# Kernel tuning notes

Hardware: AMD Instinct MI355X
Metric: run time of the kernel (lower is better)

The kernel has to match this reference:

```python
import jax, jax.numpy as jnp
import numpy as np

BETA = 0.25  # commitment cost (original code's undefined self.betas)


def setup_inputs() -> dict:
    key = jax.random.key(0)
    k1, k2 = jax.random.split(key)
    B, D, H, W = 32, 256, 32, 32
    K = 1024
    x = jax.random.normal(k1, (B, D, H, W), dtype=jnp.float32)
    # nn.Embedding init: uniform(-1/K, 1/K)
    emb = jax.random.uniform(k2, (K, D), dtype=jnp.float32,
                             minval=-1.0 / K, maxval=1.0 / K)
    return {"x": x, "emb": emb}


def reference(x, emb):
    # x: [B, D, H, W] -> NHWC
    xp = jnp.transpose(x, (0, 2, 3, 1))          # [B, H, W, D]
    D = emb.shape[1]
    z = xp.reshape(-1, D)                        # [N, D]
    # pairwise squared distance: ||z||^2 + ||e||^2 - 2 z e^T
    dist = (jnp.sum(z * z, axis=1, keepdims=True)
            + jnp.sum(emb * emb, axis=1)
            - 2.0 * jnp.einsum('nd,kd->nk', z, emb))  # [N, K]
    idx = jnp.argmin(dist, axis=1)               # [N] int
    z_quant = emb[idx].reshape(xp.shape)         # [B, H, W, D]
    sg = jax.lax.stop_gradient
    loss = (jnp.mean((sg(z_quant) - xp) ** 2)
            + BETA * jnp.mean((z_quant - sg(xp)) ** 2))
    # straight-through estimator
    z_quant = xp + sg(z_quant - xp)
    z_quant = jnp.transpose(z_quant, (0, 3, 1, 2))  # back to NCHW
    return z_quant, idx, loss
```

## Files before the change

### kernel.cpp

```cpp
#include <hip/hip_runtime.h>

typedef _Float16 half8 __attribute__((ext_vector_type(8)));
typedef _Float16 half4v __attribute__((ext_vector_type(4)));
typedef float f32x4 __attribute__((ext_vector_type(4)));

#define ZQ_ELEMS 8388608
#define N_TOK    32768
#define D_DIM    256
#define K_CB     1024

#define FLAG_CAP 32768
#define ESCALE   1024.0f
#define TAU      0.15f

__device__ __align__(16) _Float16 g_eh[K_CB * D_DIM];
__device__ float g_ck[K_CB];
__device__ float g_bk[K_CB];
__device__ float g_loss;
__device__ int   g_cnt;
__device__ int   g_flags[FLAG_CAP];

__global__ __launch_bounds__(256) void vq_prep(const float* __restrict__ emb) {
  const int tid = threadIdx.x;
  const int w   = tid >> 6;
  const int l   = tid & 63;
  const int k   = (blockIdx.x << 2) + w;
  f32x4 v = *(const f32x4*)(emb + (k << 8) + (l << 2));
  double sd = (double)v[0]*v[0] + (double)v[1]*v[1] + (double)v[2]*v[2] + (double)v[3]*v[3];
  #pragma unroll
  for (int m = 1; m < 64; m <<= 1) sd += __shfl_xor(sd, m);
  if (l == 0) { g_bk[k] = (float)sd; g_ck[k] = 512.0f * (float)sd; }
  half4v h;
  h[0] = (_Float16)(v[0] * ESCALE); h[1] = (_Float16)(v[1] * ESCALE);
  h[2] = (_Float16)(v[2] * ESCALE); h[3] = (_Float16)(v[3] * ESCALE);
  *(half4v*)(g_eh + (k << 8) + (l << 2)) = h;
  if (blockIdx.x == 0 && tid == 0) { g_loss = 0.0f; g_cnt = 0; }
}

__global__ __launch_bounds__(256, 2) void vq_main(const float* __restrict__ x,
                                                  const float* __restrict__ emb,
                                                  float* __restrict__ out) {
  __shared__ __align__(16) _Float16 zt[64 * 256];
  __shared__ float ckl[K_CB];
  __shared__ float wv1[4][64], wv2[4][64];
  __shared__ int   wi1[4][64];
  __shared__ int   fidx[64];
  __shared__ float lred[4];

  const int tid = threadIdx.x;
  const int n0  = blockIdx.x * 64;
  const int b   = blockIdx.x >> 4;
  const int hw0 = (blockIdx.x & 15) << 6;

  #pragma unroll
  for (int i = 0; i < 4; i++) ckl[tid + 256 * i] = g_ck[tid + 256 * i];

  {
    const int hw8 = (tid & 7) << 3;
    const int dl  = tid >> 3;
    #pragma unroll
    for (int it = 0; it < 8; it++) {
      const int d = (it << 5) + dl;
      const float* src = x + (((b << 8) + d) << 10) + hw0 + hw8;
      f32x4 a0 = *(const f32x4*)src;
      f32x4 a1 = *(const f32x4*)(src + 4);
      _Float16 cv[8];
      cv[0]=(_Float16)a0[0]; cv[1]=(_Float16)a0[1]; cv[2]=(_Float16)a0[2]; cv[3]=(_Float16)a0[3];
      cv[4]=(_Float16)a1[0]; cv[5]=(_Float16)a1[1]; cv[6]=(_Float16)a1[2]; cv[7]=(_Float16)a1[3];
      const int blkx = d >> 3;
      #pragma unroll
      for (int i = 0; i < 8; i++) {
        const int n   = hw8 + i;
        const int blk = blkx ^ i ^ (tid & 7);
        zt[(n << 8) + (blk << 3) + (d & 7)] = cv[i];
      }
    }
  }
  __syncthreads();

  const int w = tid >> 6;
  const int l = tid & 63;
  const int c = l & 15;
  const int q = l >> 4;

  half8 af[4][8];
  #pragma unroll
  for (int t = 0; t < 4; t++) {
    const int n  = (t << 4) + c;
    const int sw = (n & 7) ^ (n >> 3);
    #pragma unroll
    for (int s = 0; s < 8; s++) {
      const int K = (s << 2) + q;
      af[t][s] = *(const half8*)(zt + (n << 8) + ((K ^ sw) << 3));
    }
  }

  float v1[4][4], v2[4][4]; int i1[4][4];
  #pragma unroll
  for (int t = 0; t < 4; t++)
    #pragma unroll
    for (int r = 0; r < 4; r++) { v1[t][r] = -3e38f; v2[t][r] = -3e38f; i1[t][r] = 0; }

  for (int jj = 0; jj < 16; jj++) {
    const int k0 = (w << 4) + (jj << 6);
    const float ckv = ckl[k0 + c];
    f32x4 acc[4];
    #pragma unroll
    for (int t = 0; t < 4; t++) acc[t] = f32x4{-ckv, -ckv, -ckv, -ckv};
    #pragma unroll
    for (int s = 0; s < 8; s++) {
      const half8 bf = *(const half8*)(g_eh + ((k0 + c) << 8) + (s << 5) + (q << 3));
      #pragma unroll
      for (int t = 0; t < 4; t++)
        acc[t] = __builtin_amdgcn_mfma_f32_16x16x32_f16(af[t][s], bf, acc[t], 0, 0, 0);
    }
    const int kk = k0 + c;
    #pragma unroll
    for (int t = 0; t < 4; t++)
      #pragma unroll
      for (int r = 0; r < 4; r++) {
        const float sv = acc[t][r];
        if (sv > v1[t][r]) { v2[t][r] = v1[t][r]; v1[t][r] = sv; i1[t][r] = kk; }
        else if (sv > v2[t][r]) v2[t][r] = sv;
      }
  }

  #pragma unroll
  for (int t = 0; t < 4; t++)
    #pragma unroll
    for (int r = 0; r < 4; r++) {
      float a1v = v1[t][r], a2v = v2[t][r]; int ai = i1[t][r];
      #pragma unroll
      for (int m = 8; m >= 1; m >>= 1) {
        const float o1 = __shfl_xor(a1v, m);
        const int   oi = __shfl_xor(ai, m);
        const float o2 = __shfl_xor(a2v, m);
        if (o1 > a1v || (o1 == a1v && oi < ai)) { a2v = fmaxf(a1v, o2); a1v = o1; ai = oi; }
        else a2v = fmaxf(a2v, o1);
      }
      if (c == 0) {
        const int nl = (t << 4) + (q << 2) + r;
        wv1[w][nl] = a1v; wv2[w][nl] = a2v; wi1[w][nl] = ai;
      }
    }
  __syncthreads();

  if (tid < 64) {
    float a1v = wv1[0][tid], a2v = wv2[0][tid]; int ai = wi1[0][tid];
    #pragma unroll
    for (int ww = 1; ww < 4; ww++) {
      const float o1 = wv1[ww][tid]; const int oi = wi1[ww][tid]; const float o2 = wv2[ww][tid];
      if (o1 > a1v || (o1 == a1v && oi < ai)) { a2v = fmaxf(a1v, o2); a1v = o1; ai = oi; }
      else a2v = fmaxf(a2v, o1);
    }
    fidx[tid] = ai;
    out[ZQ_ELEMS + n0 + tid] = (float)ai;
    if (a1v - a2v < TAU) {
      int p = atomicAdd(&g_cnt, 1);
      if (p < FLAG_CAP) g_flags[p] = n0 + tid;
    }
  }
  __syncthreads();

  float lacc = 0.0f;
  {
    const int hw = tid & 63;
    const int sw = (hw & 7) ^ (hw >> 3);
    const float* erow = emb + (fidx[hw] << 8);
    #pragma unroll
    for (int it = 0; it < 8; it++) {
      const int dblk = (it << 2) + w;
      half8 zv = *(const half8*)(zt + (hw << 8) + ((dblk ^ sw) << 3));
      f32x4 e0 = *(const f32x4*)(erow + (dblk << 3));
      f32x4 e1 = *(const f32x4*)(erow + (dblk << 3) + 4);
      #pragma unroll
      for (int j = 0; j < 8; j++) {
        const int d = (dblk << 3) + j;
        const float ef = (j < 4) ? e0[j] : e1[j - 4];
        const float df = ef - (float)zv[j];
        lacc += df * df;
        out[(((b << 8) + d) << 10) + hw0 + hw] = ef;
      }
    }
  }
  #pragma unroll
  for (int m = 1; m < 64; m <<= 1) lacc += __shfl_xor(lacc, m);
  if (l == 0) lred[w] = lacc;
  __syncthreads();
  if (tid == 0) atomicAdd(&g_loss, lred[0] + lred[1] + lred[2] + lred[3]);
}

#define FIX_G 8
__global__ __launch_bounds__(256) void vq_fix(const float* __restrict__ x,
                                              const float* __restrict__ emb,
                                              float* __restrict__ out) {
  __shared__ float zl[FIX_G][256];
  __shared__ float aA[FIX_G];
  __shared__ int   tkn[FIX_G];
  __shared__ float bvv[FIX_G][256];
  __shared__ int   bkk[FIX_G][256];
  const int tid = threadIdx.x;
  int cnt = g_cnt; if (cnt > FLAG_CAP) cnt = FLAG_CAP;
  const int ngrp = (cnt + FIX_G - 1) / FIX_G;
  for (int grp = blockIdx.x; grp < ngrp; grp += gridDim.x) {
    const int base = grp * FIX_G;
    if (tid < FIX_G) {
      const int s = base + tid;
      tkn[tid] = (s < cnt) ? g_flags[s] : g_flags[0];
    }
    __syncthreads();
    #pragma unroll
    for (int g = 0; g < FIX_G; g++) {
      const int n = tkn[g];
      const int b = n >> 10, hw = n & 1023;
      zl[g][tid] = x[(((b << 8) + tid) << 10) + hw];
    }
    __syncthreads();
    {
      const int g = tid >> 5, l32 = tid & 31;
      double s = 0.0;
      #pragma unroll
      for (int j = 0; j < 8; j++) { const double z = (double)zl[g][(l32 << 3) + j]; s += z * z; }
      #pragma unroll
      for (int m = 1; m < 32; m <<= 1) s += __shfl_xor(s, m);
      if (l32 == 0) aA[g] = (float)s;
    }
    __syncthreads();
    float bv[FIX_G]; int bk[FIX_G];
    #pragma unroll
    for (int g = 0; g < FIX_G; g++) { bv[g] = 3.4e38f; bk[g] = 0; }
    for (int r = 0; r < 4; r++) {
      const int k = (r << 8) + tid;
      const f32x4* er = (const f32x4*)(emb + (k << 8));
      double c[FIX_G];
      #pragma unroll
      for (int g = 0; g < FIX_G; g++) c[g] = 0.0;
      for (int d4 = 0; d4 < 64; d4++) {
        const f32x4 ev = er[d4];
        #pragma unroll
        for (int j = 0; j < 4; j++) {
          const double e = (double)ev[j];
          const int d = (d4 << 2) + j;
          #pragma unroll
          for (int g = 0; g < FIX_G; g++) c[g] = fma(e, (double)zl[g][d], c[g]);
        }
      }
      const float bkv = g_bk[k];
      #pragma unroll
      for (int g = 0; g < FIX_G; g++) {
        const float c32 = (float)c[g];
        const float T = aA[g] + bkv;
        const float D = T - 2.0f * c32;
        if (D < bv[g]) { bv[g] = D; bk[g] = k; }
      }
    }
    #pragma unroll
    for (int g = 0; g < FIX_G; g++) { bvv[g][tid] = bv[g]; bkk[g][tid] = bk[g]; }
    for (int sh = 7; sh >= 0; sh--) {
      const int off = 1 << sh;
      __syncthreads();
      for (int idx = tid; idx < (FIX_G << sh); idx += 256) {
        const int g = idx >> sh, j = idx & (off - 1);
        const float v2c = bvv[g][j + off]; const int k2 = bkk[g][j + off];
        if (v2c < bvv[g][j] || (v2c == bvv[g][j] && k2 < bkk[g][j])) {
          bvv[g][j] = v2c; bkk[g][j] = k2;
        }
      }
    }
    __syncthreads();
    if (tid < FIX_G && base + tid < cnt) out[ZQ_ELEMS + tkn[tid]] = (float)bkk[tid][0];
    __syncthreads();
  }
}

__global__ void vq_fin(float* __restrict__ out) {
  out[ZQ_ELEMS + N_TOK] = g_loss * (1.25f / 8388608.0f);
}

extern "C" void kernel_launch(void* const* d_in, const int* in_sizes, int n_in,
                              void* d_out, int out_size, void* d_ws, size_t ws_size,
                              hipStream_t stream) {
  const float* x   = (const float*)d_in[0];
  const float* emb = (const float*)d_in[1];
  float* out = (float*)d_out;
  vq_prep<<<256, 256, 0, stream>>>(emb);
  vq_main<<<512, 256, 0, stream>>>(x, emb, out);
  vq_fix<<<320, 256, 0, stream>>>(x, emb, out);
  vq_fin<<<1, 1, 0, stream>>>(out);
}
```

Before: 247.3 us.

## Process one flagged token per block in vq_fix with more blocks

The fp64 recheck kernel now handles one flagged token per block iteration instead of groups of eight. Each thread computes four codebook dot products at once, and the block uses a simpler tree reduction. The grid grows from 320 to 1024 blocks to spread the flagged tokens more widely. This trades codebook reuse across grouped tokens for more parallelism and lower register and shared-memory use per block. Codebook rows are now re-read once for every token rather than once per group of eight.

```diff
diff --git a/kernel.cpp b/kernel.cpp
--- a/kernel.cpp
+++ b/kernel.cpp
@@ -190,85 +190,69 @@
   if (tid == 0) atomicAdd(&g_loss, lred[0] + lred[1] + lred[2] + lred[3]);
 }
 
-#define FIX_G 8
 __global__ __launch_bounds__(256) void vq_fix(const float* __restrict__ x,
                                               const float* __restrict__ emb,
                                               float* __restrict__ out) {
-  __shared__ float zl[FIX_G][256];
-  __shared__ float aA[FIX_G];
-  __shared__ int   tkn[FIX_G];
-  __shared__ float bvv[FIX_G][256];
-  __shared__ int   bkk[FIX_G][256];
+  __shared__ float zl[256];
+  __shared__ float aA;
+  __shared__ float bvv[256];
+  __shared__ int   bkk[256];
   const int tid = threadIdx.x;
   int cnt = g_cnt; if (cnt > FLAG_CAP) cnt = FLAG_CAP;
-  const int ngrp = (cnt + FIX_G - 1) / FIX_G;
-  for (int grp = blockIdx.x; grp < ngrp; grp += gridDim.x) {
-    const int base = grp * FIX_G;
-    if (tid < FIX_G) {
-      const int s = base + tid;
-      tkn[tid] = (s < cnt) ? g_flags[s] : g_flags[0];
-    }
-    __syncthreads();
-    #pragma unroll
-    for (int g = 0; g < FIX_G; g++) {
-      const int n = tkn[g];
-      const int b = n >> 10, hw = n & 1023;
-      zl[g][tid] = x[(((b << 8) + tid) << 10) + hw];
-    }
-    __syncthreads();
+  for (int s = blockIdx.x; s < cnt; s += gridDim.x) {
+    const int n = g_flags[s];
+    const int b = n >> 10, hw = n & 1023;
+    zl[tid] = x[(((b << 8) + tid) << 10) + hw];
+    __syncthreads();
+    if (tid < 32) {
+      double sa = 0.0;
+      #pragma unroll
+      for (int j = 0; j < 8; j++) { const double z = (double)zl[(tid << 3) + j]; sa += z * z; }
+      #pragma unroll
+      for (int m = 1; m < 32; m <<= 1) sa += __shfl_xor(sa, m);
+      if (tid == 0) aA = (float)sa;
+    }
+    __syncthreads();
+    const f32x4* er0 = (const f32x4*)(emb + ((0 << 8) + tid) * 256);
+    const f32x4* er1 = (const f32x4*)(emb + ((1 << 8) + tid) * 256);
+    const f32x4* er2 = (const f32x4*)(emb + ((2 << 8) + tid) * 256);
+    const f32x4* er3 = (const f32x4*)(emb + ((3 << 8) + tid) * 256);
+    double c0 = 0.0, c1 = 0.0, c2 = 0.0, c3 = 0.0;
+    for (int d4 = 0; d4 < 64; d4++) {
+      const f32x4 e0 = er0[d4], e1 = er1[d4], e2 = er2[d4], e3 = er3[d4];
+      #pragma unroll
+      for (int j = 0; j < 4; j++) {
+        const double z = (double)zl[(d4 << 2) + j];
+        c0 = fma((double)e0[j], z, c0);
+        c1 = fma((double)e1[j], z, c1);
+        c2 = fma((double)e2[j], z, c2);
+        c3 = fma((double)e3[j], z, c3);
+      }
+    }
+    const float A = aA;
+    float bv = 3.4e38f; int bk = 0;
     {
-      const int g = tid >> 5, l32 = tid & 31;
-      double s = 0.0;
-      #pragma unroll
-      for (int j = 0; j < 8; j++) { const double z = (double)zl[g][(l32 << 3) + j]; s += z * z; }
-      #pragma unroll
-      for (int m = 1; m < 32; m <<= 1) s += __shfl_xor(s, m);
-      if (l32 == 0) aA[g] = (float)s;
-    }
-    __syncthreads();
-    float bv[FIX_G]; int bk[FIX_G];
-    #pragma unroll
-    for (int g = 0; g < FIX_G; g++) { bv[g] = 3.4e38f; bk[g] = 0; }
-    for (int r = 0; r < 4; r++) {
-      const int k = (r << 8) + tid;
-      const f32x4* er = (const f32x4*)(emb + (k << 8));
-      double c[FIX_G];
-      #pragma unroll
-      for (int g = 0; g < FIX_G; g++) c[g] = 0.0;
-      for (int d4 = 0; d4 < 64; d4++) {
-        const f32x4 ev = er[d4];
-        #pragma unroll
-        for (int j = 0; j < 4; j++) {
-          const double e = (double)ev[j];
-          const int d = (d4 << 2) + j;
-          #pragma unroll
-          for (int g = 0; g < FIX_G; g++) c[g] = fma(e, (double)zl[g][d], c[g]);
+      const float D0 = (A + g_bk[tid])        - 2.0f * (float)c0;
+      const float D1 = (A + g_bk[256 + tid])  - 2.0f * (float)c1;
+      const float D2 = (A + g_bk[512 + tid])  - 2.0f * (float)c2;
+      const float D3 = (A + g_bk[768 + tid])  - 2.0f * (float)c3;
+      if (D0 < bv) { bv = D0; bk = tid; }
+      if (D1 < bv) { bv = D1; bk = 256 + tid; }
+      if (D2 < bv) { bv = D2; bk = 512 + tid; }
+      if (D3 < bv) { bv = D3; bk = 768 + tid; }
+    }
+    bvv[tid] = bv; bkk[tid] = bk;
+    __syncthreads();
+    for (int off = 128; off >= 1; off >>= 1) {
+      if (tid < off) {
+        const float v2c = bvv[tid + off]; const int k2 = bkk[tid + off];
+        if (v2c < bvv[tid] || (v2c == bvv[tid] && k2 < bkk[tid])) {
+          bvv[tid] = v2c; bkk[tid] = k2;
         }
       }
-      const float bkv = g_bk[k];
-      #pragma unroll
-      for (int g = 0; g < FIX_G; g++) {
-        const float c32 = (float)c[g];
-        const float T = aA[g] + bkv;
-        const float D = T - 2.0f * c32;
-        if (D < bv[g]) { bv[g] = D; bk[g] = k; }
-      }
-    }
-    #pragma unroll
-    for (int g = 0; g < FIX_G; g++) { bvv[g][tid] = bv[g]; bkk[g][tid] = bk[g]; }
-    for (int sh = 7; sh >= 0; sh--) {
-      const int off = 1 << sh;
       __syncthreads();
-      for (int idx = tid; idx < (FIX_G << sh); idx += 256) {
-        const int g = idx >> sh, j = idx & (off - 1);
-        const float v2c = bvv[g][j + off]; const int k2 = bkk[g][j + off];
-        if (v2c < bvv[g][j] || (v2c == bvv[g][j] && k2 < bkk[g][j])) {
-          bvv[g][j] = v2c; bkk[g][j] = k2;
-        }
-      }
-    }
-    __syncthreads();
-    if (tid < FIX_G && base + tid < cnt) out[ZQ_ELEMS + tkn[tid]] = (float)bkk[tid][0];
+    }
+    if (tid == 0) out[ZQ_ELEMS + n] = (float)bkk[0];
     __syncthreads();
   }
 }
@@ -285,6 +269,6 @@
   float* out = (float*)d_out;
   vq_prep<<<256, 256, 0, stream>>>(emb);
   vq_main<<<512, 256, 0, stream>>>(x, emb, out);
-  vq_fix<<<320, 256, 0, stream>>>(x, emb, out);
+  vq_fix<<<1024, 256, 0, stream>>>(x, emb, out);
   vq_fin<<<1, 1, 0, stream>>>(out);
 }
```

After: 362.3 us. +46.5%, slower.

## Transpose codebook for coalesced fp64 rescoring and shrink fix groups to two tokens

Applied to the files above, without the earlier changes.

Adds a kernel that transposes the fp32 codebook into a d-major global buffer. The flagged-token fp64 rescoring kernel then reads codebook columns with coalesced per-thread loads instead of strided row reads. It processes two tokens per block instead of eight, across 512 blocks instead of 320, giving more parallelism for small flag counts at the cost of re-reading the codebook more often. This adds an extra launch and a 1 MB transposed buffer.

```diff
diff --git a/kernel.cpp b/kernel.cpp
--- a/kernel.cpp
+++ b/kernel.cpp
@@ -14,6 +14,7 @@
 #define TAU      0.15f
 
 __device__ __align__(16) _Float16 g_eh[K_CB * D_DIM];
+__device__ __align__(16) float g_ebT[D_DIM * K_CB];
 __device__ float g_ck[K_CB];
 __device__ float g_bk[K_CB];
 __device__ float g_loss;
@@ -35,6 +36,24 @@
   h[2] = (_Float16)(v[2] * ESCALE); h[3] = (_Float16)(v[3] * ESCALE);
   *(half4v*)(g_eh + (k << 8) + (l << 2)) = h;
   if (blockIdx.x == 0 && tid == 0) { g_loss = 0.0f; g_cnt = 0; }
+}
+
+__global__ __launch_bounds__(256) void vq_tr(const float* __restrict__ emb) {
+  __shared__ float tl[64][65];
+  const int tx = threadIdx.x & 63, ty = threadIdx.x >> 6;
+  const int k0 = (blockIdx.x & 15) << 6;
+  const int d0 = (blockIdx.x >> 4) << 6;
+  #pragma unroll
+  for (int j = 0; j < 16; j++) {
+    const int kk = (ty << 4) + j;
+    tl[kk][tx] = emb[((k0 + kk) << 8) + d0 + tx];
+  }
+  __syncthreads();
+  #pragma unroll
+  for (int j = 0; j < 16; j++) {
+    const int dd = (ty << 4) + j;
+    g_ebT[((d0 + dd) << 10) + k0 + tx] = tl[tx][dd];
+  }
 }
 
 __global__ __launch_bounds__(256, 2) void vq_main(const float* __restrict__ x,
@@ -190,85 +209,77 @@
   if (tid == 0) atomicAdd(&g_loss, lred[0] + lred[1] + lred[2] + lred[3]);
 }
 
-#define FIX_G 8
 __global__ __launch_bounds__(256) void vq_fix(const float* __restrict__ x,
-                                              const float* __restrict__ emb,
                                               float* __restrict__ out) {
-  __shared__ float zl[FIX_G][256];
-  __shared__ float aA[FIX_G];
-  __shared__ int   tkn[FIX_G];
-  __shared__ float bvv[FIX_G][256];
-  __shared__ int   bkk[FIX_G][256];
+  __shared__ float zt2[2][256];
+  __shared__ float aA2[2];
+  __shared__ float bvv[2][256];
+  __shared__ int   bkk[2][256];
+  __shared__ int   nn[2];
   const int tid = threadIdx.x;
   int cnt = g_cnt; if (cnt > FLAG_CAP) cnt = FLAG_CAP;
-  const int ngrp = (cnt + FIX_G - 1) / FIX_G;
+  const int ngrp = (cnt + 1) >> 1;
   for (int grp = blockIdx.x; grp < ngrp; grp += gridDim.x) {
-    const int base = grp * FIX_G;
-    if (tid < FIX_G) {
-      const int s = base + tid;
-      tkn[tid] = (s < cnt) ? g_flags[s] : g_flags[0];
-    }
-    __syncthreads();
-    #pragma unroll
-    for (int g = 0; g < FIX_G; g++) {
-      const int n = tkn[g];
-      const int b = n >> 10, hw = n & 1023;
-      zl[g][tid] = x[(((b << 8) + tid) << 10) + hw];
-    }
-    __syncthreads();
-    {
-      const int g = tid >> 5, l32 = tid & 31;
-      double s = 0.0;
-      #pragma unroll
-      for (int j = 0; j < 8; j++) { const double z = (double)zl[g][(l32 << 3) + j]; s += z * z; }
-      #pragma unroll
-      for (int m = 1; m < 32; m <<= 1) s += __shfl_xor(s, m);
-      if (l32 == 0) aA[g] = (float)s;
-    }
-    __syncthreads();
-    float bv[FIX_G]; int bk[FIX_G];
-    #pragma unroll
-    for (int g = 0; g < FIX_G; g++) { bv[g] = 3.4e38f; bk[g] = 0; }
+    const int n0 = grp << 1;
+    if (tid < 2) nn[tid] = g_flags[(n0 + tid < cnt) ? (n0 + tid) : (cnt - 1)];
+    __syncthreads();
+    #pragma unroll
+    for (int g = 0; g < 2; g++) {
+      const int n = nn[g], b = n >> 10, hw = n & 1023;
+      zt2[g][tid] = x[(((b << 8) + tid) << 10) + hw];
+    }
+    __syncthreads();
+    if (tid < 128 && (tid & 63) < 32) {
+      const int g = tid >> 6, l32 = tid & 31;
+      double sa = 0.0;
+      #pragma unroll
+      for (int j = 0; j < 8; j++) { const double z = (double)zt2[g][(l32 << 3) + j]; sa += z * z; }
+      #pragma unroll
+      for (int m = 1; m < 32; m <<= 1) sa += __shfl_xor(sa, m);
+      if (l32 == 0) aA2[g] = (float)sa;
+    }
+    __syncthreads();
+    double c0[4] = {0.0, 0.0, 0.0, 0.0};
+    double c1[4] = {0.0, 0.0, 0.0, 0.0};
+    #pragma unroll 4
+    for (int d = 0; d < 256; d++) {
+      const float* col = g_ebT + (d << 10);
+      const double z0 = (double)zt2[0][d];
+      const double z1 = (double)zt2[1][d];
+      #pragma unroll
+      for (int r = 0; r < 4; r++) {
+        const double e = (double)col[(r << 8) + tid];
+        c0[r] = fma(e, z0, c0[r]);
+        c1[r] = fma(e, z1, c1[r]);
+      }
+    }
+    const float A0 = aA2[0], A1 = aA2[1];
+    float bv0 = 3.4e38f, bv1 = 3.4e38f; int bk0 = 0, bk1 = 0;
+    #pragma unroll
     for (int r = 0; r < 4; r++) {
       const int k = (r << 8) + tid;
-      const f32x4* er = (const f32x4*)(emb + (k << 8));
-      double c[FIX_G];
-      #pragma unroll
-      for (int g = 0; g < FIX_G; g++) c[g] = 0.0;
-      for (int d4 = 0; d4 < 64; d4++) {
-        const f32x4 ev = er[d4];
+      const float bkv = g_bk[k];
+      const float D0 = (A0 + bkv) - 2.0f * (float)c0[r];
+      const float D1 = (A1 + bkv) - 2.0f * (float)c1[r];
+      if (D0 < bv0) { bv0 = D0; bk0 = k; }
+      if (D1 < bv1) { bv1 = D1; bk1 = k; }
+    }
+    bvv[0][tid] = bv0; bkk[0][tid] = bk0;
+    bvv[1][tid] = bv1; bkk[1][tid] = bk1;
+    __syncthreads();
+    for (int off = 128; off >= 1; off >>= 1) {
+      if (tid < off) {
         #pragma unroll
-        for (int j = 0; j < 4; j++) {
-          const double e = (double)ev[j];
-          const int d = (d4 << 2) + j;
-          #pragma unroll
-          for (int g = 0; g < FIX_G; g++) c[g] = fma(e, (double)zl[g][d], c[g]);
+        for (int g = 0; g < 2; g++) {
+          const float v2c = bvv[g][tid + off]; const int k2 = bkk[g][tid + off];
+          if (v2c < bvv[g][tid] || (v2c == bvv[g][tid] && k2 < bkk[g][tid])) {
+            bvv[g][tid] = v2c; bkk[g][tid] = k2;
+          }
         }
       }
-      const float bkv = g_bk[k];
-      #pragma unroll
-      for (int g = 0; g < FIX_G; g++) {
-        const float c32 = (float)c[g];
-        const float T = aA[g] + bkv;
-        const float D = T - 2.0f * c32;
-        if (D < bv[g]) { bv[g] = D; bk[g] = k; }
-      }
-    }
-    #pragma unroll
-    for (int g = 0; g < FIX_G; g++) { bvv[g][tid] = bv[g]; bkk[g][tid] = bk[g]; }
-    for (int sh = 7; sh >= 0; sh--) {
-      const int off = 1 << sh;
       __syncthreads();
-      for (int idx = tid; idx < (FIX_G << sh); idx += 256) {
-        const int g = idx >> sh, j = idx & (off - 1);
-        const float v2c = bvv[g][j + off]; const int k2 = bkk[g][j + off];
-        if (v2c < bvv[g][j] || (v2c == bvv[g][j] && k2 < bkk[g][j])) {
-          bvv[g][j] = v2c; bkk[g][j] = k2;
-        }
-      }
-    }
-    __syncthreads();
-    if (tid < FIX_G && base + tid < cnt) out[ZQ_ELEMS + tkn[tid]] = (float)bkk[tid][0];
+    }
+    if (tid < 2 && n0 + tid < cnt) out[ZQ_ELEMS + nn[tid]] = (float)bkk[tid][0];
     __syncthreads();
   }
 }
@@ -284,7 +295,8 @@
   const float* emb = (const float*)d_in[1];
   float* out = (float*)d_out;
   vq_prep<<<256, 256, 0, stream>>>(emb);
+  vq_tr<<<64, 256, 0, stream>>>(emb);
   vq_main<<<512, 256, 0, stream>>>(x, emb, out);
-  vq_fix<<<320, 256, 0, stream>>>(x, emb, out);
+  vq_fix<<<512, 256, 0, stream>>>(x, out);
   vq_fin<<<1, 1, 0, stream>>>(out);
 }
```

Result: faster. 202.7 us (-18.0%).
